# Performance work log

Hardware: AMD Instinct MI355X
Metric: run time of the kernel (lower is better)

Reference implementation:

```python
import jax, jax.numpy as jnp
import numpy as np
from jax.ops import segment_sum

IN_DIM, HID_DIM, OUT_DIM = 128, 128, 64
N_NODES, N_EDGES = 50000, 800000


def gcn_conv(x, src, dst, W, b, n_nodes):
    # Symmetric GCN normalization (no self loops): deg at targets from unit weights
    deg = segment_sum(jnp.ones(src.shape[0], dtype=x.dtype), dst, num_segments=n_nodes)
    dinv = jnp.where(deg > 0, jax.lax.rsqrt(jnp.maximum(deg, 1.0)), 0.0)
    norm = dinv[src] * dinv[dst]                      # [E]
    h = x @ W                                         # [N, out] small GEMM first (PyG order)
    msg = h[src] * norm[:, None]                      # gather + scale: [E, out]
    out = segment_sum(msg, dst, num_segments=n_nodes) # scatter-add to targets
    return out + b


def setup_inputs() -> dict:
    key = jax.random.key(0)
    k1, k2, k3, k4, k5 = jax.random.split(key, 5)
    x = jax.random.normal(k1, (N_NODES, IN_DIM), dtype=jnp.float32)
    edge_index = jax.random.randint(k2, (2, N_EDGES), 0, N_NODES, dtype=jnp.int64)
    s1 = 1.0 / np.sqrt(IN_DIM)
    s2 = 1.0 / np.sqrt(HID_DIM)
    W1 = jax.random.uniform(k3, (IN_DIM, HID_DIM), jnp.float32, -s1, s1)
    b1 = jnp.zeros((HID_DIM,), jnp.float32)
    W2 = jax.random.uniform(k4, (HID_DIM, OUT_DIM), jnp.float32, -s2, s2)
    b2 = jnp.zeros((OUT_DIM,), jnp.float32)
    return {"x": x, "edge_index": edge_index, "W1": W1, "b1": b1, "W2": W2, "b2": b2}


def reference(x, edge_index, W1, b1, W2, b2):
    n_nodes = x.shape[0]
    src, dst = edge_index[0], edge_index[1]
    h = gcn_conv(x, src, dst, W1, b1, n_nodes)
    h = jax.nn.relu(h)
    # Dropout is identity in eval mode (reference is deterministic)
    out = gcn_conv(h, src, dst, W2, b2, n_nodes)
    return out
```

## Files before the change

### kernel.cpp

```cpp
#include <hip/hip_runtime.h>

#define N_NODES 50000
#define N_EDGES 800000
#define IN_DIM  128
#define HID_DIM 128
#define OUT_DIM 64

#define NPAD 50176
#define NB 7
#define KEYS (N_NODES * NB)
#define KPAD 350208
#define NB_SCAN2 (KPAD / 1024)
#define FILLB ((N_EDGES / 4 + 255) / 256)
#define GEMM1B ((N_NODES + 63) / 64)
#define DINVB ((N_NODES + 1023) / 1024)

typedef __attribute__((ext_vector_type(8))) short bf16x8;
typedef __attribute__((ext_vector_type(4))) float f32x4;

__device__ __forceinline__ unsigned short f2bf(float f) {
    unsigned u = __float_as_uint(f);
    u += 0x7fffu + ((u >> 16) & 1u);
    return (unsigned short)(u >> 16);
}
__device__ __forceinline__ float bflo(unsigned u) { return __uint_as_float(u << 16); }
__device__ __forceinline__ float bfhi(unsigned u) { return __uint_as_float(u & 0xffff0000u); }

#define ACC8(u)  do { \
    acc[0] += bflo(u.x); acc[1] += bfhi(u.x); \
    acc[2] += bflo(u.y); acc[3] += bfhi(u.y); \
    acc[4] += bflo(u.z); acc[5] += bfhi(u.z); \
    acc[6] += bflo(u.w); acc[7] += bfhi(u.w); } while (0)


__global__ void rank_hist_kernel(const int* __restrict__ src, const int* __restrict__ dst,
                                 int* __restrict__ cnt2, int* __restrict__ rank) {
    int e = blockIdx.x * 256 + threadIdx.x;
    if (e >= N_EDGES) return;
    int s = src[e], d = dst[e];
    rank[e] = atomicAdd(&cnt2[d * NB + (s >> 13)], 1);
}


__global__ __launch_bounds__(1024) void prep_kernel(const int* __restrict__ cnt2,
                                                    int* __restrict__ blockSums,
                                                    float* __restrict__ dinv,
                                                    const float* __restrict__ W1,
                                                    const float* __restrict__ W2,
                                                    unsigned short* __restrict__ w1t,
                                                    unsigned short* __restrict__ w2t) {
    int bid = blockIdx.x;
    if (bid < NB_SCAN2) {
        __shared__ int s[1024];
        int i = bid * 1024 + threadIdx.x;
        s[threadIdx.x] = (i < KEYS) ? cnt2[i] : 0;
        __syncthreads();
        for (int off = 512; off > 0; off >>= 1) {
            if (threadIdx.x < off) s[threadIdx.x] += s[threadIdx.x + off];
            __syncthreads();
        }
        if (threadIdx.x == 0) blockSums[bid] = s[0];
    } else if (bid < NB_SCAN2 + DINVB) {
        int d = (bid - NB_SCAN2) * 1024 + threadIdx.x;
        if (d < N_NODES) {
            int base = d * NB;
            int deg = cnt2[base] + cnt2[base + 1] + cnt2[base + 2] + cnt2[base + 3]
                    + cnt2[base + 4] + cnt2[base + 5] + cnt2[base + 6];
            dinv[d] = (deg > 0) ? rsqrtf((float)deg) : 0.0f;
        }
    } else if (bid < NB_SCAN2 + DINVB + 4) {
        int idx = (bid - NB_SCAN2 - DINVB) * 1024 + threadIdx.x;
        int c = idx >> 5, k4 = (idx & 31) * 4;
        ushort4 o;
        o.x = f2bf(W1[(k4 + 0) * 128 + c]);
        o.y = f2bf(W1[(k4 + 1) * 128 + c]);
        o.z = f2bf(W1[(k4 + 2) * 128 + c]);
        o.w = f2bf(W1[(k4 + 3) * 128 + c]);
        *(ushort4*)(w1t + c * 128 + k4) = o;
    } else {
        int idx = (bid - NB_SCAN2 - DINVB - 4) * 1024 + threadIdx.x;
        if (idx >= 64 * 32) return;
        int c = idx >> 5, k4 = (idx & 31) * 4;
        ushort4 o;
        o.x = f2bf(W2[(k4 + 0) * 64 + c]);
        o.y = f2bf(W2[(k4 + 1) * 64 + c]);
        o.z = f2bf(W2[(k4 + 2) * 64 + c]);
        o.w = f2bf(W2[(k4 + 3) * 64 + c]);
        *(ushort4*)(w2t + c * 128 + k4) = o;
    }
}


__global__ __launch_bounds__(1024) void scan_kernel(const int* __restrict__ cnt2,
                                                    const int* __restrict__ blockSums,
                                                    int* __restrict__ rs) {
    __shared__ int s[1024];
    __shared__ int sums[NB_SCAN2];
    __shared__ int base_s;
    if (threadIdx.x < NB_SCAN2) sums[threadIdx.x] = blockSums[threadIdx.x];
    if (blockIdx.x == 0 && threadIdx.x == 0) rs[KEYS] = N_EDGES;
    int i = blockIdx.x * 1024 + threadIdx.x;
    int v = (i < KEYS) ? cnt2[i] : 0;
    s[threadIdx.x] = v;
    __syncthreads();
    if (threadIdx.x == 0) {
        int run = 0;
        for (int b = 0; b < (int)blockIdx.x; ++b) run += sums[b];
        base_s = run;
    }
    for (int off = 1; off < 1024; off <<= 1) {
        int t = (threadIdx.x >= off) ? s[threadIdx.x - off] : 0;
        __syncthreads();
        s[threadIdx.x] += t;
        __syncthreads();
    }
    if (i < KEYS) rs[i] = base_s + s[threadIdx.x] - v;
}


__global__ __launch_bounds__(256) void fill_gemm1_kernel(const int* __restrict__ src,
                                                         const int* __restrict__ dst,
                                                         const int* __restrict__ rank,
                                                         const int* __restrict__ rs,
                                                         int* __restrict__ csr_src,
                                                         const float* __restrict__ x,
                                                         const unsigned short* __restrict__ w1t,
                                                         const float* __restrict__ dinv,
                                                         unsigned short* __restrict__ h1b) {
    int bid = blockIdx.x;
    if (bid < FILLB) {
        int e = (bid * 256 + threadIdx.x) * 4;
        if (e >= N_EDGES) return;
        int4 s4 = *(const int4*)(src + e);
        int4 d4 = *(const int4*)(dst + e);
        int4 r4 = *(const int4*)(rank + e);
        csr_src[rs[d4.x * NB + (s4.x >> 13)] + r4.x] = s4.x;
        csr_src[rs[d4.y * NB + (s4.y >> 13)] + r4.y] = s4.y;
        csr_src[rs[d4.z * NB + (s4.z >> 13)] + r4.z] = s4.z;
        csr_src[rs[d4.w * NB + (s4.w >> 13)] + r4.w] = s4.w;
        return;
    }

    int gb = bid - FILLB;
    int wave = threadIdx.x >> 6;
    int lane = threadIdx.x & 63;
    int n = lane & 15, quad = lane >> 4;
    int row0 = gb * 64 + wave * 16;

    int arow = row0 + n;
    if (arow >= N_NODES) arow = N_NODES - 1;
    const float* aptr = x + (size_t)arow * 128 + quad * 8;
    const unsigned short* bbase = w1t + (size_t)n * 128 + quad * 8;

    f32x4 acc[8];
#pragma unroll
    for (int t = 0; t < 8; ++t) acc[t] = (f32x4){0.f, 0.f, 0.f, 0.f};

#pragma unroll
    for (int w4 = 0; w4 < 4; ++w4) {
        float4 f0 = *(const float4*)(aptr + w4 * 32);
        float4 f1 = *(const float4*)(aptr + w4 * 32 + 4);
        bf16x8 af;
        af[0] = (short)f2bf(f0.x); af[1] = (short)f2bf(f0.y);
        af[2] = (short)f2bf(f0.z); af[3] = (short)f2bf(f0.w);
        af[4] = (short)f2bf(f1.x); af[5] = (short)f2bf(f1.y);
        af[6] = (short)f2bf(f1.z); af[7] = (short)f2bf(f1.w);
#pragma unroll
        for (int t = 0; t < 8; ++t) {
            bf16x8 bf = *(const bf16x8*)(bbase + (size_t)t * 2048 + w4 * 32);
            acc[t] = __builtin_amdgcn_mfma_f32_16x16x32_bf16(af, bf, acc[t], 0, 0, 0);
        }
    }

#pragma unroll
    for (int r = 0; r < 4; ++r) {
        int row = row0 + quad * 4 + r;
        if (row < N_NODES) {
            float dn = dinv[row];
            unsigned short* o = h1b + (size_t)row * 128 + n;
#pragma unroll
            for (int t = 0; t < 8; ++t) o[t * 16] = f2bf(acc[t][r] * dn);
        }
    }
}


#define A1T_STRIDE 136

__global__ __launch_bounds__(256) void agg1_gemm2_fused(const int* __restrict__ csr_src,
                                                        const int* __restrict__ rs,
                                                        const float* __restrict__ dinv,
                                                        const float* __restrict__ b1,
                                                        const unsigned short* __restrict__ h1b,
                                                        const unsigned short* __restrict__ w2t,
                                                        unsigned short* __restrict__ h2b) {
    __shared__ unsigned short a1t[16 * A1T_STRIDE];

    int node0 = blockIdx.x * 16;
    int g = threadIdx.x >> 4;
    int q = threadIdx.x & 15;
    int node = node0 + g;
    int start = rs[node * NB];
    int m = rs[node * NB + NB] - start;

    float acc[8] = {};
    int j = 0;
    for (; j + 3 < m; j += 4) {
        int s0 = csr_src[start + j];
        int s1 = csr_src[start + j + 1];
        int s2 = csr_src[start + j + 2];
        int s3 = csr_src[start + j + 3];
        uint4 u0 = ((const uint4*)(h1b + (size_t)s0 * 128))[q];
        uint4 u1 = ((const uint4*)(h1b + (size_t)s1 * 128))[q];
        uint4 u2 = ((const uint4*)(h1b + (size_t)s2 * 128))[q];
        uint4 u3 = ((const uint4*)(h1b + (size_t)s3 * 128))[q];
        ACC8(u0); ACC8(u1); ACC8(u2); ACC8(u3);
    }
    for (; j < m; ++j) {
        int s0 = csr_src[start + j];
        uint4 u0 = ((const uint4*)(h1b + (size_t)s0 * 128))[q];
        ACC8(u0);
    }

    {
        float dn = dinv[node];
        float4 bA = ((const float4*)b1)[2 * q];
        float4 bB = ((const float4*)b1)[2 * q + 1];
        ushort4 oA, oB;
        oA.x = f2bf(fmaxf(acc[0] * dn + bA.x, 0.f));
        oA.y = f2bf(fmaxf(acc[1] * dn + bA.y, 0.f));
        oA.z = f2bf(fmaxf(acc[2] * dn + bA.z, 0.f));
        oA.w = f2bf(fmaxf(acc[3] * dn + bA.w, 0.f));
        oB.x = f2bf(fmaxf(acc[4] * dn + bB.x, 0.f));
        oB.y = f2bf(fmaxf(acc[5] * dn + bB.y, 0.f));
        oB.z = f2bf(fmaxf(acc[6] * dn + bB.z, 0.f));
        oB.w = f2bf(fmaxf(acc[7] * dn + bB.w, 0.f));
        ushort4* o = (ushort4*)(a1t + g * A1T_STRIDE + q * 8);
        o[0] = oA;
        o[1] = oB;
    }
    __syncthreads();

    int wave = threadIdx.x >> 6;
    int lane = threadIdx.x & 63;
    int n = lane & 15, quad = lane >> 4;
    const unsigned short* bbase = w2t + (size_t)(wave * 16 + n) * 128 + quad * 8;
    const unsigned short* abase = a1t + (size_t)n * A1T_STRIDE + quad * 8;

    f32x4 c2 = (f32x4){0.f, 0.f, 0.f, 0.f};
#pragma unroll
    for (int w4 = 0; w4 < 4; ++w4) {
        bf16x8 af = *(const bf16x8*)(abase + w4 * 32);
        bf16x8 bf = *(const bf16x8*)(bbase + w4 * 32);
        c2 = __builtin_amdgcn_mfma_f32_16x16x32_bf16(af, bf, c2, 0, 0, 0);
    }

#pragma unroll
    for (int r = 0; r < 4; ++r) {
        int row = node0 + quad * 4 + r;
        float dn = dinv[row];
        h2b[(size_t)row * 64 + wave * 16 + n] = f2bf(c2[r] * dn);
    }
}


__global__ __launch_bounds__(256) void agg2_kernel(const int* __restrict__ csr_src,
                                                   const int* __restrict__ rs,
                                                   const float* __restrict__ dinv,
                                                   const float* __restrict__ b2,
                                                   const unsigned short* __restrict__ h2b,
                                                   float* __restrict__ out) {
    int node = blockIdx.x * 4 + (threadIdx.x >> 6);
    if (node >= N_NODES) return;
    int lane = threadIdx.x & 63;
    int grp = lane >> 3;
    int q   = lane & 7;
    int start = rs[node * NB];
    int m = rs[node * NB + NB] - start;

    float acc[8] = {};

    int j = grp;
    for (; j + 8 < m; j += 16) {
        int s0 = csr_src[start + j];
        int s1 = csr_src[start + j + 8];
        uint4 u0 = ((const uint4*)(h2b + (size_t)s0 * 64))[q];
        uint4 u1 = ((const uint4*)(h2b + (size_t)s1 * 64))[q];
        ACC8(u0); ACC8(u1);
    }
    if (j < m) {
        int s0 = csr_src[start + j];
        uint4 u0 = ((const uint4*)(h2b + (size_t)s0 * 64))[q];
        ACC8(u0);
    }

#pragma unroll
    for (int d = 8; d <= 32; d <<= 1) {
#pragma unroll
        for (int c = 0; c < 8; ++c) acc[c] += __shfl_xor(acc[c], d, 64);
    }

    if (lane < 8) {
        float dn = dinv[node];
        float4 bA = ((const float4*)b2)[2 * q];
        float4 bB = ((const float4*)b2)[2 * q + 1];
        float4 rA, rB;
        rA.x = acc[0] * dn + bA.x;
        rA.y = acc[1] * dn + bA.y;
        rA.z = acc[2] * dn + bA.z;
        rA.w = acc[3] * dn + bA.w;
        rB.x = acc[4] * dn + bB.x;
        rB.y = acc[5] * dn + bB.y;
        rB.z = acc[6] * dn + bB.z;
        rB.w = acc[7] * dn + bB.w;
        float4* o = (float4*)(out + (size_t)node * 64);
        o[2 * q] = rA;
        o[2 * q + 1] = rB;
    }
}


extern "C" void kernel_launch(void* const* d_in, const int* in_sizes, int n_in,
                              void* d_out, int out_size, void* d_ws, size_t ws_size,
                              hipStream_t stream) {
    const float* x  = (const float*)d_in[0];
    const int*   ei = (const int*)d_in[1];
    const float* W1 = (const float*)d_in[2];
    const float* b1 = (const float*)d_in[3];
    const float* W2 = (const float*)d_in[4];
    const float* b2 = (const float*)d_in[5];
    float* out = (float*)d_out;

    const int* src = ei;
    const int* dst = ei + N_EDGES;

    char* ws = (char*)d_ws;
    int*   cnt2      = (int*)ws;
    int*   rs        = cnt2 + KPAD;
    int*   blockSums = rs + KPAD;
    float* dinv      = (float*)(blockSums + 384);
    int*   rank      = (int*)(dinv + NPAD);
    int*   csr_src   = rank + N_EDGES;
    unsigned short* h1b = (unsigned short*)(csr_src + N_EDGES);
    unsigned short* h2b = h1b + (size_t)N_NODES * HID_DIM;
    unsigned short* w1t = h2b + (size_t)N_NODES * OUT_DIM;
    unsigned short* w2t = w1t + 128 * 128;

    hipMemsetAsync(cnt2, 0, KPAD * sizeof(int), stream);

    rank_hist_kernel<<<(N_EDGES + 255) / 256, 256, 0, stream>>>(src, dst, cnt2, rank);

    prep_kernel<<<NB_SCAN2 + DINVB + 6, 1024, 0, stream>>>(cnt2, blockSums, dinv,
                                                           W1, W2, w1t, w2t);

    scan_kernel<<<NB_SCAN2, 1024, 0, stream>>>(cnt2, blockSums, rs);

    fill_gemm1_kernel<<<FILLB + GEMM1B, 256, 0, stream>>>(src, dst, rank, rs, csr_src,
                                                          x, w1t, dinv, h1b);

    agg1_gemm2_fused<<<N_NODES / 16, 256, 0, stream>>>(csr_src, rs, dinv, b1, h1b, w2t, h2b);

    agg2_kernel<<<(N_NODES + 3) / 4, 256, 0, stream>>>(csr_src, rs, dinv, b2, h2b, out);
}
```

Baseline: 207.2 us.

## Fuse prefix scan into prep kernel using single-pass cross-block lookback

Replaces the two-kernel scan (block-sum reduction in the prep kernel, then a separate scan kernel) with one kernel. Each block scans its own tile, publishes its total through an atomic flag array, and spin-waits on the totals of all earlier blocks to get its offset. This removes one kernel launch and the re-read of the histogram. In exchange it depends on all scan blocks being co-resident to avoid deadlock, and adds spin-wait traffic on global atomics.

```diff
diff --git a/kernel.cpp b/kernel.cpp
--- a/kernel.cpp
+++ b/kernel.cpp
@@ -42,26 +42,46 @@
 }
 
 
-__global__ __launch_bounds__(1024) void prep_kernel(const int* __restrict__ cnt2,
-                                                    int* __restrict__ blockSums,
-                                                    float* __restrict__ dinv,
-                                                    const float* __restrict__ W1,
-                                                    const float* __restrict__ W2,
-                                                    unsigned short* __restrict__ w1t,
-                                                    unsigned short* __restrict__ w2t) {
+__global__ __launch_bounds__(1024) void scan_all_kernel(const int* __restrict__ cnt2,
+                                                        int* __restrict__ partials,
+                                                        int* __restrict__ rs,
+                                                        float* __restrict__ dinv,
+                                                        const float* __restrict__ W1,
+                                                        const float* __restrict__ W2,
+                                                        unsigned short* __restrict__ w1t,
+                                                        unsigned short* __restrict__ w2t) {
     int bid = blockIdx.x;
+    int tid = threadIdx.x;
     if (bid < NB_SCAN2) {
         __shared__ int s[1024];
-        int i = bid * 1024 + threadIdx.x;
-        s[threadIdx.x] = (i < KEYS) ? cnt2[i] : 0;
+        __shared__ int p[1024];
+        int i = bid * 1024 + tid;
+        int v = (i < KEYS) ? cnt2[i] : 0;
+        s[tid] = v;
+        __syncthreads();
+        for (int off = 1; off < 1024; off <<= 1) {
+            int t = (tid >= off) ? s[tid - off] : 0;
+            __syncthreads();
+            s[tid] += t;
+            __syncthreads();
+        }
+        if (tid == 0) atomicExch(&partials[bid], s[1023] + 1);
+        if (bid == 0 && tid == 0) rs[KEYS] = N_EDGES;
+        int myp = 0;
+        if (tid < bid) {
+            int val;
+            do { val = atomicAdd(&partials[tid], 0); } while (val == 0);
+            myp = val - 1;
+        }
+        p[tid] = myp;
         __syncthreads();
         for (int off = 512; off > 0; off >>= 1) {
-            if (threadIdx.x < off) s[threadIdx.x] += s[threadIdx.x + off];
+            if (tid < off) p[tid] += p[tid + off];
             __syncthreads();
         }
-        if (threadIdx.x == 0) blockSums[bid] = s[0];
+        if (i < KEYS) rs[i] = p[0] + s[tid] - v;
     } else if (bid < NB_SCAN2 + DINVB) {
-        int d = (bid - NB_SCAN2) * 1024 + threadIdx.x;
+        int d = (bid - NB_SCAN2) * 1024 + tid;
         if (d < N_NODES) {
             int base = d * NB;
             int deg = cnt2[base] + cnt2[base + 1] + cnt2[base + 2] + cnt2[base + 3]
@@ -69,7 +89,7 @@
             dinv[d] = (deg > 0) ? rsqrtf((float)deg) : 0.0f;
         }
     } else if (bid < NB_SCAN2 + DINVB + 4) {
-        int idx = (bid - NB_SCAN2 - DINVB) * 1024 + threadIdx.x;
+        int idx = (bid - NB_SCAN2 - DINVB) * 1024 + tid;
         int c = idx >> 5, k4 = (idx & 31) * 4;
         ushort4 o;
         o.x = f2bf(W1[(k4 + 0) * 128 + c]);
@@ -78,8 +98,7 @@
         o.w = f2bf(W1[(k4 + 3) * 128 + c]);
         *(ushort4*)(w1t + c * 128 + k4) = o;
     } else {
-        int idx = (bid - NB_SCAN2 - DINVB - 4) * 1024 + threadIdx.x;
-        if (idx >= 64 * 32) return;
+        int idx = (bid - NB_SCAN2 - DINVB - 4) * 1024 + tid;
         int c = idx >> 5, k4 = (idx & 31) * 4;
         ushort4 o;
         o.x = f2bf(W2[(k4 + 0) * 64 + c]);
@@ -88,33 +107,6 @@
         o.w = f2bf(W2[(k4 + 3) * 64 + c]);
         *(ushort4*)(w2t + c * 128 + k4) = o;
     }
-}
-
-
-__global__ __launch_bounds__(1024) void scan_kernel(const int* __restrict__ cnt2,
-                                                    const int* __restrict__ blockSums,
-                                                    int* __restrict__ rs) {
-    __shared__ int s[1024];
-    __shared__ int sums[NB_SCAN2];
-    __shared__ int base_s;
-    if (threadIdx.x < NB_SCAN2) sums[threadIdx.x] = blockSums[threadIdx.x];
-    if (blockIdx.x == 0 && threadIdx.x == 0) rs[KEYS] = N_EDGES;
-    int i = blockIdx.x * 1024 + threadIdx.x;
-    int v = (i < KEYS) ? cnt2[i] : 0;
-    s[threadIdx.x] = v;
-    __syncthreads();
-    if (threadIdx.x == 0) {
-        int run = 0;
-        for (int b = 0; b < (int)blockIdx.x; ++b) run += sums[b];
-        base_s = run;
-    }
-    for (int off = 1; off < 1024; off <<= 1) {
-        int t = (threadIdx.x >= off) ? s[threadIdx.x - off] : 0;
-        __syncthreads();
-        s[threadIdx.x] += t;
-        __syncthreads();
-    }
-    if (i < KEYS) rs[i] = base_s + s[threadIdx.x] - v;
 }
 
 
@@ -336,9 +328,9 @@
 
     char* ws = (char*)d_ws;
     int*   cnt2      = (int*)ws;
-    int*   rs        = cnt2 + KPAD;
-    int*   blockSums = rs + KPAD;
-    float* dinv      = (float*)(blockSums + 384);
+    int*   partials  = cnt2 + KPAD;
+    int*   rs        = partials + 512;
+    float* dinv      = (float*)(rs + KPAD);
     int*   rank      = (int*)(dinv + NPAD);
     int*   csr_src   = rank + N_EDGES;
     unsigned short* h1b = (unsigned short*)(csr_src + N_EDGES);
@@ -346,14 +338,12 @@
     unsigned short* w1t = h2b + (size_t)N_NODES * OUT_DIM;
     unsigned short* w2t = w1t + 128 * 128;
 
-    hipMemsetAsync(cnt2, 0, KPAD * sizeof(int), stream);
+    hipMemsetAsync(cnt2, 0, (KPAD + 512) * sizeof(int), stream);
 
     rank_hist_kernel<<<(N_EDGES + 255) / 256, 256, 0, stream>>>(src, dst, cnt2, rank);
 
-    prep_kernel<<<NB_SCAN2 + DINVB + 6, 1024, 0, stream>>>(cnt2, blockSums, dinv,
-                                                           W1, W2, w1t, w2t);
-
-    scan_kernel<<<NB_SCAN2, 1024, 0, stream>>>(cnt2, blockSums, rs);
+    scan_all_kernel<<<NB_SCAN2 + DINVB + 6, 1024, 0, stream>>>(cnt2, partials, rs, dinv,
+                                                               W1, W2, w1t, w2t);
 
     fill_gemm1_kernel<<<FILLB + GEMM1B, 256, 0, stream>>>(src, dst, rank, rs, csr_src,
                                                           x, w1t, dinv, h1b);
```

After: 204.7 us. Within noise of the previous version (-1.2%).
